# Kernel tuning notes

Hardware: AMD Instinct MI355X
Metric: run time of the kernel (lower is better)

The kernel has to match this reference:

```python
import jax, jax.numpy as jnp
import numpy as np

B, N, F = 4, 4096, 64

def setup_inputs() -> dict:
    key = jax.random.key(0)
    ks = jax.random.split(key, 7)
    X = jax.random.normal(ks[0], (B, N, F), dtype=jnp.float32)
    A0 = jax.random.uniform(ks[1], (B, N, N), dtype=jnp.float32)
    A1 = jax.random.uniform(ks[2], (B, N, N), dtype=jnp.float32)
    A2 = jax.random.uniform(ks[3], (B, N, N), dtype=jnp.float32)
    w0 = jax.random.normal(ks[4], (F, F), dtype=jnp.float32) * 0.05
    w1 = jax.random.normal(ks[5], (F, F), dtype=jnp.float32) * 0.05
    w2 = jax.random.normal(ks[6], (F, F), dtype=jnp.float32) * 0.05
    return {"X": X, "A0": A0, "A1": A1, "A2": A2, "w0": w0, "w1": w1, "w2": w2}

def reference(X, A0, A1, A2, w0, w1, w2):
    # Three parallel (A @ X) @ W chains, summed, then ReLU.
    # bnm,bmf->bnf then bnf,fg->bng
    p0 = jnp.einsum('bnf,fg->bng', jnp.matmul(A0, X), w0)
    p1 = jnp.einsum('bnf,fg->bng', jnp.matmul(A1, X), w1)
    p2 = jnp.einsum('bnf,fg->bng', jnp.matmul(A2, X), w2)
    return jax.nn.relu(p0 + p1 + p2)
```

## Files before the change

kernel.cpp:

```cpp
#include <hip/hip_runtime.h>

#define NN 4096
#define BB 4
#define FF 64

typedef __attribute__((ext_vector_type(8))) short short8;
typedef __attribute__((ext_vector_type(4))) float f32x4;

__device__ inline unsigned short f2bf(float f) {
    unsigned int u = __float_as_uint(f);
    u += 0x7fffu + ((u >> 16) & 1u);
    return (unsigned short)(u >> 16);
}

__global__ __launch_bounds__(256) void prep_z(
    const float* __restrict__ X,
    const float* __restrict__ w0, const float* __restrict__ w1, const float* __restrict__ w2,
    unsigned short* __restrict__ Zt)
{
    __shared__ float Xs[64][68];
    __shared__ unsigned short Zts[64][72];
    const int blk = blockIdx.x;
    const int b = blk >> 6;
    const int k0 = (blk & 63) << 6;
    const int t = threadIdx.x;
    {
        const int kk = t >> 2, c4 = t & 3;
        const float* src = X + ((size_t)b * NN + k0 + kk) * FF;
        #pragma unroll
        for (int p = 0; p < 4; ++p) {
            float4 v = *(const float4*)(src + 4 * (c4 + 4 * p));
            *(float4*)&Xs[kk][4 * (c4 + 4 * p)] = v;
        }
    }
    __syncthreads();
    const int lane = t & 63, w = t >> 6;
    const float* ws[3] = {w0, w1, w2};
    for (int i = 0; i < 3; ++i) {
        float acc[16];
        #pragma unroll
        for (int j = 0; j < 16; ++j) acc[j] = 0.f;
        const float* wp = ws[i];
        for (int c = 0; c < 64; ++c) {
            float wv = wp[c * FF + lane];
            #pragma unroll
            for (int j = 0; j < 16; ++j) acc[j] += Xs[w * 16 + j][c] * wv;
        }
        __syncthreads();
        #pragma unroll
        for (int j = 0; j < 16; ++j) Zts[lane][w * 16 + j] = f2bf(acc[j]);
        __syncthreads();
        #pragma unroll
        for (int cc = 0; cc < 2; ++cc) {
            int ch = t + cc * 256;
            int f = ch >> 3, o8 = (ch & 7) * 8;
            float4 v = *(const float4*)&Zts[f][o8];
            *(float4*)(Zt + (((size_t)i * BB + b) * FF + f) * NN + k0 + o8) = v;
        }
    }
}

__global__ __launch_bounds__(768) void gnn_main(
    const float* __restrict__ A0, const float* __restrict__ A1, const float* __restrict__ A2,
    const unsigned short* __restrict__ Zt,
    float* __restrict__ out)
{
    __shared__ unsigned short lds[3 * 2 * 64 * 72];
    const int blk = blockIdx.x;
    const int b = blk >> 6;
    const int m0 = (blk & 63) << 6;
    const int t = threadIdx.x;
    const int lane = t & 63;
    const int wave = t >> 6;
    const int ig = wave >> 2;
    const int w4 = wave & 3;
    const int gtid = t & 255;

    const float* Ai = (ig == 0) ? A0 : (ig == 1) ? A1 : A2;
    unsigned short* As = lds + ig * (2 * 64 * 72);
    unsigned short* Zs = As + 64 * 72;

    const int r = gtid >> 2, c4 = gtid & 3;
    const float* Abase = Ai + (size_t)b * NN * NN + (size_t)(m0 + r) * NN;
    const int zf0 = gtid >> 3, zo0 = (gtid & 7) * 8;
    const int zf1 = (gtid + 256) >> 3, zo1 = ((gtid + 256) & 7) * 8;
    const unsigned short* Zbase = Zt + (((size_t)ig * BB + b) * FF) * NN;
    const unsigned short* Zp0 = Zbase + (size_t)zf0 * NN + zo0;
    const unsigned short* Zp1 = Zbase + (size_t)zf1 * NN + zo1;

    f32x4 acc[4] = {};

    float4 apf[4];
    float4 zpf0, zpf1;
    #pragma unroll
    for (int p = 0; p < 4; ++p) apf[p] = *(const float4*)(Abase + 4 * c4 + 16 * p);
    zpf0 = *(const float4*)Zp0;
    zpf1 = *(const float4*)Zp1;

    const unsigned short* Arow = As + (w4 * 16 + (lane & 15)) * 72 + (lane >> 4) * 8;
    const unsigned short* Zrow = Zs + (lane & 15) * 72 + (lane >> 4) * 8;

    for (int step = 0; step < 64; ++step) {
        __syncthreads();
        #pragma unroll
        for (int p = 0; p < 4; ++p) {
            ushort4 u;
            u.x = f2bf(apf[p].x); u.y = f2bf(apf[p].y);
            u.z = f2bf(apf[p].z); u.w = f2bf(apf[p].w);
            *(ushort4*)(As + r * 72 + 4 * c4 + 16 * p) = u;
        }
        *(float4*)(Zs + zf0 * 72 + zo0) = zpf0;
        *(float4*)(Zs + zf1 * 72 + zo1) = zpf1;
        if (step < 63) {
            const float* Ab = Abase + (step + 1) * 64;
            #pragma unroll
            for (int p = 0; p < 4; ++p) apf[p] = *(const float4*)(Ab + 4 * c4 + 16 * p);
            zpf0 = *(const float4*)(Zp0 + (step + 1) * 64);
            zpf1 = *(const float4*)(Zp1 + (step + 1) * 64);
        }
        __syncthreads();
        #pragma unroll
        for (int kh = 0; kh < 2; ++kh) {
            short8 af = *(const short8*)(Arow + kh * 32);
            #pragma unroll
            for (int nt = 0; nt < 4; ++nt) {
                short8 bf = *(const short8*)(Zrow + nt * 16 * 72 + kh * 32);
                acc[nt] = __builtin_amdgcn_mfma_f32_16x16x32_bf16(af, bf, acc[nt], 0, 0, 0);
            }
        }
    }

    __syncthreads();
    float* Cred = (float*)lds;
    for (int g = 0; g < 3; ++g) {
        if (ig == g) {
            #pragma unroll
            for (int nt = 0; nt < 4; ++nt) {
                #pragma unroll
                for (int j = 0; j < 4; ++j) {
                    int row = w4 * 16 + (lane >> 4) * 4 + j;
                    int col = nt * 16 + (lane & 15);
                    if (g == 0) Cred[row * 68 + col] = acc[nt][j];
                    else        Cred[row * 68 + col] += acc[nt][j];
                }
            }
        }
        __syncthreads();
    }
    if (ig == 0) {
        float* orow = out + ((size_t)b * NN + m0 + r) * FF;
        #pragma unroll
        for (int p = 0; p < 4; ++p) {
            int c0 = 4 * (c4 + 4 * p);
            float4 v = *(const float4*)&Cred[r * 68 + c0];
            v.x = fmaxf(v.x, 0.f); v.y = fmaxf(v.y, 0.f);
            v.z = fmaxf(v.z, 0.f); v.w = fmaxf(v.w, 0.f);
            *(float4*)(orow + c0) = v;
        }
    }
}

extern "C" void kernel_launch(void* const* d_in, const int* in_sizes, int n_in,
                              void* d_out, int out_size, void* d_ws, size_t ws_size,
                              hipStream_t stream) {
    const float* X  = (const float*)d_in[0];
    const float* A0 = (const float*)d_in[1];
    const float* A1 = (const float*)d_in[2];
    const float* A2 = (const float*)d_in[3];
    const float* w0 = (const float*)d_in[4];
    const float* w1 = (const float*)d_in[5];
    const float* w2 = (const float*)d_in[6];
    float* out = (float*)d_out;
    unsigned short* Zt = (unsigned short*)d_ws;

    prep_z<<<256, 256, 0, stream>>>(X, w0, w1, w2, Zt);
    gnn_main<<<256, 768, 0, stream>>>(A0, A1, A2, Zt, out);
}
```

Baseline: 788.6 us.

## Rewrite GNN kernels with LDS-free direct-load MFMA and split-K across waves

The main kernel drops the shared-memory staging of A and Z and the barriers inside the loop. Each wave loads A rows and bf16 Z directly from global memory into registers and runs 32x32x16 bf16 MFMAs over a quarter of the K range, accumulating all three adjacency chains into one accumulator. The partial results are reduced through LDS at the end, and the grid becomes 512 blocks of 32 rows with two blocks per CU. The prep kernel also switches to MFMA for X@W. Reads are now per-lane strided rather than coalesced tile loads, and there is no software prefetch pipeline, so performance depends on the hardware hiding memory latency.

```diff
diff --git a/kernel.cpp b/kernel.cpp
--- a/kernel.cpp
+++ b/kernel.cpp
@@ -2,10 +2,9 @@
 
 #define NN 4096
 #define BB 4
-#define FF 64
 
 typedef __attribute__((ext_vector_type(8))) short short8;
-typedef __attribute__((ext_vector_type(4))) float f32x4;
+typedef __attribute__((ext_vector_type(16))) float f32x16;
 
 __device__ inline unsigned short f2bf(float f) {
     unsigned int u = __float_as_uint(f);
@@ -18,145 +17,126 @@
     const float* __restrict__ w0, const float* __restrict__ w1, const float* __restrict__ w2,
     unsigned short* __restrict__ Zt)
 {
-    __shared__ float Xs[64][68];
-    __shared__ unsigned short Zts[64][72];
     const int blk = blockIdx.x;
     const int b = blk >> 6;
     const int k0 = (blk & 63) << 6;
-    const int t = threadIdx.x;
-    {
-        const int kk = t >> 2, c4 = t & 3;
-        const float* src = X + ((size_t)b * NN + k0 + kk) * FF;
+    const int t = threadIdx.x, lane = t & 63, w = t >> 6;
+    const int f0 = (w & 1) << 5;
+    const int kw = k0 + ((w >> 1) << 5);
+    const int l31 = lane & 31;
+    const int lg = (lane >> 5) << 3;
+
+    short8 bx[4];
+    const float* xp = X + ((size_t)b * NN + kw + l31) * 64 + lg;
+    #pragma unroll
+    for (int c = 0; c < 4; ++c) {
+        float4 x0 = *(const float4*)(xp + c * 16);
+        float4 x1 = *(const float4*)(xp + c * 16 + 4);
+        bx[c][0] = (short)f2bf(x0.x); bx[c][1] = (short)f2bf(x0.y);
+        bx[c][2] = (short)f2bf(x0.z); bx[c][3] = (short)f2bf(x0.w);
+        bx[c][4] = (short)f2bf(x1.x); bx[c][5] = (short)f2bf(x1.y);
+        bx[c][6] = (short)f2bf(x1.z); bx[c][7] = (short)f2bf(x1.w);
+    }
+    const float* ws_[3] = {w0, w1, w2};
+    #pragma unroll
+    for (int i = 0; i < 3; ++i) {
+        const float* wp = ws_[i];
+        f32x16 acc = {};
         #pragma unroll
-        for (int p = 0; p < 4; ++p) {
-            float4 v = *(const float4*)(src + 4 * (c4 + 4 * p));
-            *(float4*)&Xs[kk][4 * (c4 + 4 * p)] = v;
+        for (int c = 0; c < 4; ++c) {
+            short8 aw;
+            #pragma unroll
+            for (int j = 0; j < 8; ++j)
+                aw[j] = (short)f2bf(wp[(c * 16 + lg + j) * 64 + f0 + l31]);
+            acc = __builtin_amdgcn_mfma_f32_32x32x16_bf16(aw, bx[c], acc, 0, 0, 0);
         }
-    }
-    __syncthreads();
-    const int lane = t & 63, w = t >> 6;
-    const float* ws[3] = {w0, w1, w2};
-    for (int i = 0; i < 3; ++i) {
-        float acc[16];
+        unsigned short* zp = Zt + (((size_t)i * BB + b) * 64) * NN;
         #pragma unroll
-        for (int j = 0; j < 16; ++j) acc[j] = 0.f;
-        const float* wp = ws[i];
-        for (int c = 0; c < 64; ++c) {
-            float wv = wp[c * FF + lane];
-            #pragma unroll
-            for (int j = 0; j < 16; ++j) acc[j] += Xs[w * 16 + j][c] * wv;
-        }
-        __syncthreads();
-        #pragma unroll
-        for (int j = 0; j < 16; ++j) Zts[lane][w * 16 + j] = f2bf(acc[j]);
-        __syncthreads();
-        #pragma unroll
-        for (int cc = 0; cc < 2; ++cc) {
-            int ch = t + cc * 256;
-            int f = ch >> 3, o8 = (ch & 7) * 8;
-            float4 v = *(const float4*)&Zts[f][o8];
-            *(float4*)(Zt + (((size_t)i * BB + b) * FF + f) * NN + k0 + o8) = v;
+        for (int j = 0; j < 16; ++j) {
+            int f = f0 + (j & 3) + ((j >> 2) << 3) + ((lane >> 5) << 2);
+            zp[(size_t)f * NN + kw + l31] = f2bf(acc[j]);
         }
     }
 }
 
-__global__ __launch_bounds__(768) void gnn_main(
+__global__ __launch_bounds__(256, 2) void gnn_main(
     const float* __restrict__ A0, const float* __restrict__ A1, const float* __restrict__ A2,
     const unsigned short* __restrict__ Zt,
     float* __restrict__ out)
 {
-    __shared__ unsigned short lds[3 * 2 * 64 * 72];
+    __shared__ float red[4 * 32 * 64];
     const int blk = blockIdx.x;
-    const int b = blk >> 6;
-    const int m0 = (blk & 63) << 6;
+    const int b = blk >> 7;
+    const int m0 = (blk & 127) << 5;
     const int t = threadIdx.x;
     const int lane = t & 63;
-    const int wave = t >> 6;
-    const int ig = wave >> 2;
-    const int w4 = wave & 3;
-    const int gtid = t & 255;
+    const int w = t >> 6;
 
-    const float* Ai = (ig == 0) ? A0 : (ig == 1) ? A1 : A2;
-    unsigned short* As = lds + ig * (2 * 64 * 72);
-    unsigned short* Zs = As + 64 * 72;
+    const int mrow = lane & 31;
+    const int kgrp = (lane >> 5) << 3;
 
-    const int r = gtid >> 2, c4 = gtid & 3;
-    const float* Abase = Ai + (size_t)b * NN * NN + (size_t)(m0 + r) * NN;
-    const int zf0 = gtid >> 3, zo0 = (gtid & 7) * 8;
-    const int zf1 = (gtid + 256) >> 3, zo1 = ((gtid + 256) & 7) * 8;
-    const unsigned short* Zbase = Zt + (((size_t)ig * BB + b) * FF) * NN;
-    const unsigned short* Zp0 = Zbase + (size_t)zf0 * NN + zo0;
-    const unsigned short* Zp1 = Zbase + (size_t)zf1 * NN + zo1;
+    const size_t Aoff = (size_t)b * NN * NN + (size_t)(m0 + mrow) * NN + kgrp;
+    const float* pA[3] = {A0 + Aoff, A1 + Aoff, A2 + Aoff};
+    const unsigned short* pZ[3][2];
+    #pragma unroll
+    for (int i = 0; i < 3; ++i)
+        #pragma unroll
+        for (int nt = 0; nt < 2; ++nt)
+            pZ[i][nt] = Zt + (((size_t)i * BB + b) * 64 + nt * 32 + mrow) * NN + kgrp;
 
-    f32x4 acc[4] = {};
+    f32x16 acc0 = {}, acc1 = {};
 
-    float4 apf[4];
-    float4 zpf0, zpf1;
-    #pragma unroll
-    for (int p = 0; p < 4; ++p) apf[p] = *(const float4*)(Abase + 4 * c4 + 16 * p);
-    zpf0 = *(const float4*)Zp0;
-    zpf1 = *(const float4*)Zp1;
-
-    const unsigned short* Arow = As + (w4 * 16 + (lane & 15)) * 72 + (lane >> 4) * 8;
-    const unsigned short* Zrow = Zs + (lane & 15) * 72 + (lane >> 4) * 8;
-
-    for (int step = 0; step < 64; ++step) {
-        __syncthreads();
+    const int kbeg = w << 10;
+    for (int k = kbeg; k < kbeg + 1024; k += 32) {
+        float4 a[3][2][2];
+        short8 zb[3][2][2];
         #pragma unroll
-        for (int p = 0; p < 4; ++p) {
-            ushort4 u;
-            u.x = f2bf(apf[p].x); u.y = f2bf(apf[p].y);
-            u.z = f2bf(apf[p].z); u.w = f2bf(apf[p].w);
-            *(ushort4*)(As + r * 72 + 4 * c4 + 16 * p) = u;
-        }
-        *(float4*)(Zs + zf0 * 72 + zo0) = zpf0;
-        *(float4*)(Zs + zf1 * 72 + zo1) = zpf1;
-        if (step < 63) {
-            const float* Ab = Abase + (step + 1) * 64;
+        for (int u = 0; u < 2; ++u) {
+            const int kk = k + u * 16;
             #pragma unroll
-            for (int p = 0; p < 4; ++p) apf[p] = *(const float4*)(Ab + 4 * c4 + 16 * p);
-            zpf0 = *(const float4*)(Zp0 + (step + 1) * 64);
-            zpf1 = *(const float4*)(Zp1 + (step + 1) * 64);
-        }
-        __syncthreads();
-        #pragma unroll
-        for (int kh = 0; kh < 2; ++kh) {
-            short8 af = *(const short8*)(Arow + kh * 32);
-            #pragma unroll
-            for (int nt = 0; nt < 4; ++nt) {
-                short8 bf = *(const short8*)(Zrow + nt * 16 * 72 + kh * 32);
-                acc[nt] = __builtin_amdgcn_mfma_f32_16x16x32_bf16(af, bf, acc[nt], 0, 0, 0);
+            for (int i = 0; i < 3; ++i) {
+                const float* ap = pA[i] + kk;
+                a[i][u][0] = *(const float4*)ap;
+                a[i][u][1] = *(const float4*)(ap + 4);
+                zb[i][u][0] = *(const short8*)(pZ[i][0] + kk);
+                zb[i][u][1] = *(const short8*)(pZ[i][1] + kk);
             }
         }
+        #pragma unroll
+        for (int u = 0; u < 2; ++u)
+            #pragma unroll
+            for (int i = 0; i < 3; ++i) {
+                short8 af;
+                af[0] = (short)f2bf(a[i][u][0].x); af[1] = (short)f2bf(a[i][u][0].y);
+                af[2] = (short)f2bf(a[i][u][0].z); af[3] = (short)f2bf(a[i][u][0].w);
+                af[4] = (short)f2bf(a[i][u][1].x); af[5] = (short)f2bf(a[i][u][1].y);
+                af[6] = (short)f2bf(a[i][u][1].z); af[7] = (short)f2bf(a[i][u][1].w);
+                acc0 = __builtin_amdgcn_mfma_f32_32x32x16_bf16(af, zb[i][u][0], acc0, 0, 0, 0);
+                acc1 = __builtin_amdgcn_mfma_f32_32x32x16_bf16(af, zb[i][u][1], acc1, 0, 0, 0);
+            }
     }
 
+    float* myred = red + w * 2048;
+    #pragma unroll
+    for (int j = 0; j < 16; ++j) {
+        int row = (j & 3) + ((j >> 2) << 3) + ((lane >> 5) << 2);
+        myred[row * 64 + mrow] = acc0[j];
+        myred[row * 64 + 32 + mrow] = acc1[j];
+    }
     __syncthreads();
-    float* Cred = (float*)lds;
-    for (int g = 0; g < 3; ++g) {
-        if (ig == g) {
-            #pragma unroll
-            for (int nt = 0; nt < 4; ++nt) {
-                #pragma unroll
-                for (int j = 0; j < 4; ++j) {
-                    int row = w4 * 16 + (lane >> 4) * 4 + j;
-                    int col = nt * 16 + (lane & 15);
-                    if (g == 0) Cred[row * 68 + col] = acc[nt][j];
-                    else        Cred[row * 68 + col] += acc[nt][j];
-                }
-            }
+    float* obase = out + ((size_t)b * NN + m0) * 64;
+    const int e = t * 8;
+    #pragma unroll
+    for (int p = 0; p < 2; ++p) {
+        float4 s = {0.f, 0.f, 0.f, 0.f};
+        #pragma unroll
+        for (int ww = 0; ww < 4; ++ww) {
+            float4 v = *(const float4*)(red + ww * 2048 + e + p * 4);
+            s.x += v.x; s.y += v.y; s.z += v.z; s.w += v.w;
         }
-        __syncthreads();
-    }
-    if (ig == 0) {
-        float* orow = out + ((size_t)b * NN + m0 + r) * FF;
-        #pragma unroll
-        for (int p = 0; p < 4; ++p) {
-            int c0 = 4 * (c4 + 4 * p);
-            float4 v = *(const float4*)&Cred[r * 68 + c0];
-            v.x = fmaxf(v.x, 0.f); v.y = fmaxf(v.y, 0.f);
-            v.z = fmaxf(v.z, 0.f); v.w = fmaxf(v.w, 0.f);
-            *(float4*)(orow + c0) = v;
-        }
+        s.x = fmaxf(s.x, 0.f); s.y = fmaxf(s.y, 0.f);
+        s.z = fmaxf(s.z, 0.f); s.w = fmaxf(s.w, 0.f);
+        *(float4*)(obase + e + p * 4) = s;
     }
 }
 
@@ -174,5 +154,5 @@
     unsigned short* Zt = (unsigned short*)d_ws;
 
     prep_z<<<256, 256, 0, stream>>>(X, w0, w1, w2, Zt);
-    gnn_main<<<256, 768, 0, stream>>>(A0, A1, A2, Zt, out);
+    gnn_main<<<512, 256, 0, stream>>>(A0, A1, A2, Zt, out);
 }
```

Result: slower. 830.6 us (+5.3%).
